# Kernel optimization log

Measured on AMD Instinct MI355X. Metric: run time of the kernel, lower is better.

## Reference

```python
import jax, jax.numpy as jnp
import numpy as np

MAX_ANTS = 16  # padded max draws per (batch, neuron); ragged draws masked with -1
BS, N_IN, N_OUT = 32, 4096, 4096


def setup_inputs() -> dict:
    key = jax.random.key(0)
    k1, k2 = jax.random.split(key)
    # integer ant counts per (batch, input neuron), in [0, MAX_ANTS)
    x = jax.random.randint(k1, (BS, N_IN), 0, MAX_ANTS, dtype=jnp.int32)
    # positive weights (original init is uniform 1/n_outputs; random positive is general)
    weights = jax.random.uniform(k2, (N_IN, N_OUT), dtype=jnp.float32, minval=0.01, maxval=1.0)
    return {"x": x, "weights": weights}


def reference(x, weights):
    """Vectorized equivalent of ACOLayer.forward.

    Original: for each batch b and input neuron i with count c = x[b, i] > 0,
    draw c iid categorical samples from row-normalized weights[i].
    Here: inverse-CDF sampling, padded to MAX_ANTS draws, invalid slots = -1.
    Returns int32 [bs, n_in, MAX_ANTS].
    """
    probs = weights / weights.sum(axis=1, keepdims=True)   # normalize()
    cdf = jnp.cumsum(probs, axis=1)                        # [n_in, n_out]
    bs, n_in = x.shape
    n_out = weights.shape[1]
    u = jax.random.uniform(jax.random.key(42), (bs, n_in, MAX_ANTS), dtype=weights.dtype)
    # group draws by input neuron so each row's CDF is searched once
    u_rows = u.transpose(1, 0, 2).reshape(n_in, bs * MAX_ANTS)  # [n_in, bs*MAX]
    idx = jax.vmap(jnp.searchsorted)(cdf, u_rows)               # inverse-CDF draw
    idx = jnp.minimum(idx, n_out - 1).astype(jnp.int32)
    idx = idx.reshape(n_in, bs, MAX_ANTS).transpose(1, 0, 2)    # [bs, n_in, MAX]
    valid = jnp.arange(MAX_ANTS, dtype=x.dtype)[None, None, :] < x[:, :, None]
    return jnp.where(valid, idx, -1)
```

## Files before the change

### kernel.cpp

```cpp
#include <hip/hip_runtime.h>
#include <stdint.h>


#define N_IN    4096
#define N_OUT   4096
#define BS      32
#define MAX_A   16
#define THREADS 256
#define HALF    1048576u

__device__ __forceinline__ int padi(int j) { return j + (j >> 5); }

__device__ __forceinline__ uint32_t rotl32(uint32_t x, uint32_t r) {
    return (x << r) | (x >> (32u - r));
}

__device__ __forceinline__ void threefry2x32_42(uint32_t x0, uint32_t x1,
                                                uint32_t& o0, uint32_t& o1) {
    const uint32_t k0 = 0u, k1 = 42u;
    const uint32_t k2 = k0 ^ k1 ^ 0x1BD11BDAu;
    x0 += k0; x1 += k1;
#define TF_R(r) { x0 += x1; x1 = rotl32(x1, (r)); x1 ^= x0; }
    TF_R(13) TF_R(15) TF_R(26) TF_R(6)
    x0 += k1; x1 += k2 + 1u;
    TF_R(17) TF_R(29) TF_R(16) TF_R(24)
    x0 += k2; x1 += k0 + 2u;
    TF_R(13) TF_R(15) TF_R(26) TF_R(6)
    x0 += k0; x1 += k1 + 3u;
    TF_R(17) TF_R(29) TF_R(16) TF_R(24)
    x0 += k1; x1 += k2 + 4u;
    TF_R(13) TF_R(15) TF_R(26) TF_R(6)
    x0 += k2; x1 += k0 + 5u;
#undef TF_R
    o0 = x0; o1 = x1;
}

__device__ __forceinline__ float bits_to_uniform(uint32_t b) {
    uint32_t f = (b >> 9) | 0x3f800000u;
    float r;
    __builtin_memcpy(&r, &f, 4);
    return r - 1.0f;
}

__device__ __forceinline__ int lower_bound_cdf(const float* cdf, float tval) {
    int lo = 0, hi = N_OUT;
    #pragma unroll
    for (int it = 0; it < 12; ++it) {
        int mid = (lo + hi) >> 1;
        if (cdf[padi(mid)] < tval) lo = mid + 1; else hi = mid;
    }
    return lo < N_OUT ? lo : N_OUT - 1;
}

__global__ __launch_bounds__(THREADS)
void aco_sample_kernel(const int* __restrict__ x,
                       const float* __restrict__ w,
                       int* __restrict__ out) {
    __shared__ float cdf[N_OUT + (N_OUT >> 5)];
    __shared__ float wsum[4];
    __shared__ int   xc[BS];

    const int row  = blockIdx.x;
    const int t    = threadIdx.x;
    const int lane = t & 63;
    const int wid  = t >> 6;

    const float4* wrow = (const float4*)(w + (size_t)row * N_OUT);
    float4 v0 = wrow[t * 4 + 0];
    float4 v1 = wrow[t * 4 + 1];
    float4 v2 = wrow[t * 4 + 2];
    float4 v3 = wrow[t * 4 + 3];

    if (t < BS) xc[t] = x[t * N_IN + row];

    float loc[16];
    {
        float s = 0.f;
        s += v0.x; loc[0]  = s;  s += v0.y; loc[1]  = s;
        s += v0.z; loc[2]  = s;  s += v0.w; loc[3]  = s;
        s += v1.x; loc[4]  = s;  s += v1.y; loc[5]  = s;
        s += v1.z; loc[6]  = s;  s += v1.w; loc[7]  = s;
        s += v2.x; loc[8]  = s;  s += v2.y; loc[9]  = s;
        s += v2.z; loc[10] = s;  s += v2.w; loc[11] = s;
        s += v3.x; loc[12] = s;  s += v3.y; loc[13] = s;
        s += v3.z; loc[14] = s;  s += v3.w; loc[15] = s;
    }
    const float my_total = loc[15];

    float incl = my_total;
    #pragma unroll
    for (int d = 1; d < 64; d <<= 1) {
        float n = __shfl_up(incl, d, 64);
        if (lane >= d) incl += n;
    }
    if (lane == 63) wsum[wid] = incl;
    __syncthreads();

    const float4 ws = *(const float4*)wsum;
    const float total = ws.x + ws.y + ws.z + ws.w;
    float wprefix = 0.f;
    if (wid > 0) wprefix += ws.x;
    if (wid > 1) wprefix += ws.y;
    if (wid > 2) wprefix += ws.z;
    const float chunk_prefix = wprefix + incl - my_total;

    {
        const int base = t * 16;
        #pragma unroll
        for (int m = 0; m < 16; ++m)
            cdf[padi(base + m)] = chunk_prefix + loc[m];
    }
    __syncthreads();

    const int b = t >> 4;
    const int a = t & 15;
    const uint32_t j0 = (uint32_t)(b * (N_IN * MAX_A) + row * MAX_A + a);
    const uint32_t j1 = j0 + HALF;

    uint32_t o0, o1, p0, p1;
    threefry2x32_42(0u, j0, o0, o1);
    threefry2x32_42(0u, j1, p0, p1);
    const float t0 = bits_to_uniform(o0 ^ o1) * total;
    const float t1 = bits_to_uniform(p0 ^ p1) * total;

    const int idx0 = lower_bound_cdf(cdf, t0);
    const int idx1 = lower_bound_cdf(cdf, t1);

    out[j0] = (a < xc[b])      ? idx0 : -1;
    out[j1] = (a < xc[b + 16]) ? idx1 : -1;
}

extern "C" void kernel_launch(void* const* d_in, const int* in_sizes, int n_in,
                              void* d_out, int out_size, void* d_ws, size_t ws_size,
                              hipStream_t stream) {
    const int*   x;
    const float* w;
    if (in_sizes[0] == BS * N_IN) { x = (const int*)d_in[0]; w = (const float*)d_in[1]; }
    else                          { x = (const int*)d_in[1]; w = (const float*)d_in[0]; }
    aco_sample_kernel<<<N_IN, THREADS, 0, stream>>>(x, w, (int*)d_out);
}
```

Before: 20.91 us.

## Hoist RNG before scan and guess-window binary search with fallback

Threefry random generation moves ahead of the weight prefix scan so its ALU work can overlap the global loads and block barriers. The CDF search now guesses an index from u*N_OUT, checks that the answer lies inside a ±64 window, and if so runs a 7-step search instead of 12. Otherwise it falls back to the full search, and the two draws' searches are interleaved. The window only holds when the CDF is close to uniform, which suits these near-uniform random weights. A failed check costs extra shared-memory reads and wave divergence.

```diff
diff --git a/kernel.cpp b/kernel.cpp
--- a/kernel.cpp
+++ b/kernel.cpp
@@ -8,6 +8,7 @@
 #define MAX_A   16
 #define THREADS 256
 #define HALF    1048576u
+#define WIN     64
 
 __device__ __forceinline__ int padi(int j) { return j + (j >> 5); }
 
@@ -42,16 +43,6 @@
     return r - 1.0f;
 }
 
-__device__ __forceinline__ int lower_bound_cdf(const float* cdf, float tval) {
-    int lo = 0, hi = N_OUT;
-    #pragma unroll
-    for (int it = 0; it < 12; ++it) {
-        int mid = (lo + hi) >> 1;
-        if (cdf[padi(mid)] < tval) lo = mid + 1; else hi = mid;
-    }
-    return lo < N_OUT ? lo : N_OUT - 1;
-}
-
 __global__ __launch_bounds__(THREADS)
 void aco_sample_kernel(const int* __restrict__ x,
                        const float* __restrict__ w,
@@ -72,6 +63,16 @@
     float4 v3 = wrow[t * 4 + 3];
 
     if (t < BS) xc[t] = x[t * N_IN + row];
+
+    const int bb = t >> 4;
+    const int aa = t & 15;
+    const uint32_t j0 = (uint32_t)(bb * (N_IN * MAX_A) + row * MAX_A + aa);
+    const uint32_t j1 = j0 + HALF;
+    uint32_t o0, o1, p0, p1;
+    threefry2x32_42(0u, j0, o0, o1);
+    threefry2x32_42(0u, j1, p0, p1);
+    const float u0 = bits_to_uniform(o0 ^ o1);
+    const float u1 = bits_to_uniform(p0 ^ p1);
 
     float loc[16];
     {
@@ -112,22 +113,48 @@
     }
     __syncthreads();
 
-    const int b = t >> 4;
-    const int a = t & 15;
-    const uint32_t j0 = (uint32_t)(b * (N_IN * MAX_A) + row * MAX_A + a);
-    const uint32_t j1 = j0 + HALF;
+    const float t0 = u0 * total;
+    const float t1 = u1 * total;
 
-    uint32_t o0, o1, p0, p1;
-    threefry2x32_42(0u, j0, o0, o1);
-    threefry2x32_42(0u, j1, p0, p1);
-    const float t0 = bits_to_uniform(o0 ^ o1) * total;
-    const float t1 = bits_to_uniform(p0 ^ p1) * total;
+    const int i0 = (int)(u0 * (float)N_OUT);
+    const int i1 = (int)(u1 * (float)N_OUT);
+    int lo0 = i0 - WIN; if (lo0 < 0) lo0 = 0;
+    int hi0 = i0 + WIN; if (hi0 > N_OUT) hi0 = N_OUT;
+    int lo1 = i1 - WIN; if (lo1 < 0) lo1 = 0;
+    int hi1 = i1 + WIN; if (hi1 > N_OUT) hi1 = N_OUT;
 
-    const int idx0 = lower_bound_cdf(cdf, t0);
-    const int idx1 = lower_bound_cdf(cdf, t1);
+    const bool ok0 = (lo0 == 0     || cdf[padi(lo0 - 1)] <  t0) &&
+                     (hi0 == N_OUT || cdf[padi(hi0 - 1)] >= t0);
+    const bool ok1 = (lo1 == 0     || cdf[padi(lo1 - 1)] <  t1) &&
+                     (hi1 == N_OUT || cdf[padi(hi1 - 1)] >= t1);
 
-    out[j0] = (a < xc[b])      ? idx0 : -1;
-    out[j1] = (a < xc[b + 16]) ? idx1 : -1;
+    if (ok0 && ok1) {
+        #pragma unroll
+        for (int it = 0; it < 7; ++it) {
+            const int m0 = (lo0 + hi0) >> 1;
+            const int m1 = (lo1 + hi1) >> 1;
+            const float f0 = cdf[padi(m0)];
+            const float f1 = cdf[padi(m1)];
+            if (f0 < t0) lo0 = m0 + 1; else hi0 = m0;
+            if (f1 < t1) lo1 = m1 + 1; else hi1 = m1;
+        }
+    } else {
+        lo0 = 0; hi0 = N_OUT; lo1 = 0; hi1 = N_OUT;
+        #pragma unroll
+        for (int it = 0; it < 12; ++it) {
+            const int m0 = (lo0 + hi0) >> 1;
+            const int m1 = (lo1 + hi1) >> 1;
+            const float f0 = cdf[padi(m0)];
+            const float f1 = cdf[padi(m1)];
+            if (f0 < t0) lo0 = m0 + 1; else hi0 = m0;
+            if (f1 < t1) lo1 = m1 + 1; else hi1 = m1;
+        }
+    }
+    const int idx0 = lo0 < N_OUT ? lo0 : N_OUT - 1;
+    const int idx1 = lo1 < N_OUT ? lo1 : N_OUT - 1;
+
+    out[j0] = (aa < xc[bb])      ? idx0 : -1;
+    out[j1] = (aa < xc[bb + 16]) ? idx1 : -1;
 }
 
 extern "C" void kernel_launch(void* const* d_in, const int* in_sizes, int n_in,
```

After: 19.96 us. 1.05x faster.

## Store CDF as packed fp16, halve threads, and use windowed binary search

Applied to the files above, without the earlier changes.

Halves block size to 128 threads, with each thread handling 32 weights and 4 draws. The per-row CDF is stored in shared memory as packed fp16 pairs rather than fp32. Draws are computed before the weight reduction, and the search first checks a ±64 window around the uniform-guess index, falling back to a full 12-step search. This cuts LDS footprint and search steps and raises occupancy, but fp16 CDF values (with round-toward-zero packing) lose precision, so sampled indices may differ from the fp32 reference near bucket boundaries. The window guess assumes roughly uniform weights, which holds only for the test distribution.

```diff
diff --git a/kernel.cpp b/kernel.cpp
--- a/kernel.cpp
+++ b/kernel.cpp
@@ -6,10 +6,13 @@
 #define N_OUT   4096
 #define BS      32
 #define MAX_A   16
-#define THREADS 256
+#define THREADS 128
 #define HALF    1048576u
+#define WIN     64
+#define NWORDS  (N_OUT / 2)
+#define PWORDS  (NWORDS + (NWORDS >> 5))
 
-__device__ __forceinline__ int padi(int j) { return j + (j >> 5); }
+__device__ __forceinline__ int padw(int wi) { return wi + (wi >> 5); }
 
 __device__ __forceinline__ uint32_t rotl32(uint32_t x, uint32_t r) {
     return (x << r) | (x >> (32u - r));
@@ -42,23 +45,29 @@
     return r - 1.0f;
 }
 
-__device__ __forceinline__ int lower_bound_cdf(const float* cdf, float tval) {
-    int lo = 0, hi = N_OUT;
-    #pragma unroll
-    for (int it = 0; it < 12; ++it) {
-        int mid = (lo + hi) >> 1;
-        if (cdf[padi(mid)] < tval) lo = mid + 1; else hi = mid;
-    }
-    return lo < N_OUT ? lo : N_OUT - 1;
+__device__ __forceinline__ uint32_t pack_h2(float a, float b) {
+    __fp16 v2[2];
+    *(decltype(__builtin_amdgcn_cvt_pkrtz(a, b))*)v2 = __builtin_amdgcn_cvt_pkrtz(a, b);
+    uint32_t u;
+    __builtin_memcpy(&u, v2, 4);
+    return u;
 }
 
-__global__ __launch_bounds__(THREADS)
+__device__ __forceinline__ float cdf_at(const uint32_t* cdfp, int e) {
+    const uint32_t wrd = cdfp[padw(e >> 1)];
+    const uint16_t h = (e & 1) ? (uint16_t)(wrd >> 16) : (uint16_t)(wrd & 0xffffu);
+    _Float16 v;
+    __builtin_memcpy(&v, &h, 2);
+    return (float)v;
+}
+
+__global__ __launch_bounds__(THREADS, 8)
 void aco_sample_kernel(const int* __restrict__ x,
                        const float* __restrict__ w,
                        int* __restrict__ out) {
-    __shared__ float cdf[N_OUT + (N_OUT >> 5)];
-    __shared__ float wsum[4];
-    __shared__ int   xc[BS];
+    __shared__ uint32_t cdfp[PWORDS];
+    __shared__ float    wsum[2];
+    __shared__ int      xc[BS];
 
     const int row  = blockIdx.x;
     const int t    = threadIdx.x;
@@ -66,26 +75,39 @@
     const int wid  = t >> 6;
 
     const float4* wrow = (const float4*)(w + (size_t)row * N_OUT);
-    float4 v0 = wrow[t * 4 + 0];
-    float4 v1 = wrow[t * 4 + 1];
-    float4 v2 = wrow[t * 4 + 2];
-    float4 v3 = wrow[t * 4 + 3];
+    float4 v0 = wrow[t * 8 + 0];
+    float4 v1 = wrow[t * 8 + 1];
+    float4 v2 = wrow[t * 8 + 2];
+    float4 v3 = wrow[t * 8 + 3];
+    float4 v4 = wrow[t * 8 + 4];
+    float4 v5 = wrow[t * 8 + 5];
+    float4 v6 = wrow[t * 8 + 6];
+    float4 v7 = wrow[t * 8 + 7];
 
     if (t < BS) xc[t] = x[t * N_IN + row];
 
-    float loc[16];
-    {
-        float s = 0.f;
-        s += v0.x; loc[0]  = s;  s += v0.y; loc[1]  = s;
-        s += v0.z; loc[2]  = s;  s += v0.w; loc[3]  = s;
-        s += v1.x; loc[4]  = s;  s += v1.y; loc[5]  = s;
-        s += v1.z; loc[6]  = s;  s += v1.w; loc[7]  = s;
-        s += v2.x; loc[8]  = s;  s += v2.y; loc[9]  = s;
-        s += v2.z; loc[10] = s;  s += v2.w; loc[11] = s;
-        s += v3.x; loc[12] = s;  s += v3.y; loc[13] = s;
-        s += v3.z; loc[14] = s;  s += v3.w; loc[15] = s;
+    const int bb = t >> 4;
+    const int aa = t & 15;
+    uint32_t jj[4];
+    float    uu[4];
+    #pragma unroll
+    for (int d = 0; d < 4; ++d) {
+        jj[d] = (uint32_t)((bb + 8 * d) * (N_IN * MAX_A) + row * MAX_A + aa);
+        uint32_t o0, o1;
+        threefry2x32_42(0u, jj[d], o0, o1);
+        uu[d] = bits_to_uniform(o0 ^ o1);
     }
-    const float my_total = loc[15];
+
+    float s = 0.f;
+    s += v0.x + v0.y + v0.z + v0.w;
+    s += v1.x + v1.y + v1.z + v1.w;
+    s += v2.x + v2.y + v2.z + v2.w;
+    s += v3.x + v3.y + v3.z + v3.w;
+    s += v4.x + v4.y + v4.z + v4.w;
+    s += v5.x + v5.y + v5.z + v5.w;
+    s += v6.x + v6.y + v6.z + v6.w;
+    s += v7.x + v7.y + v7.z + v7.w;
+    const float my_total = s;
 
     float incl = my_total;
     #pragma unroll
@@ -96,38 +118,68 @@
     if (lane == 63) wsum[wid] = incl;
     __syncthreads();
 
-    const float4 ws = *(const float4*)wsum;
-    const float total = ws.x + ws.y + ws.z + ws.w;
-    float wprefix = 0.f;
-    if (wid > 0) wprefix += ws.x;
-    if (wid > 1) wprefix += ws.y;
-    if (wid > 2) wprefix += ws.z;
-    const float chunk_prefix = wprefix + incl - my_total;
+    const float total = wsum[0] + wsum[1];
+    const float chunk_prefix = (wid ? wsum[0] : 0.f) + incl - my_total;
 
     {
-        const int base = t * 16;
-        #pragma unroll
-        for (int m = 0; m < 16; ++m)
-            cdf[padi(base + m)] = chunk_prefix + loc[m];
+        const int wbase = t * 16;
+        float r = chunk_prefix;
+        float f0, f1;
+#define EMIT(vv, wi_) \
+        f0 = r + vv.x; f1 = f0 + vv.y; \
+        cdfp[padw(wbase + (wi_))] = pack_h2(f0, f1); \
+        r = f1 + vv.z; f0 = r; r += vv.w; \
+        cdfp[padw(wbase + (wi_) + 1)] = pack_h2(f0, r);
+        EMIT(v0,  0) EMIT(v1,  2) EMIT(v2,  4) EMIT(v3,  6)
+        EMIT(v4,  8) EMIT(v5, 10) EMIT(v6, 12) EMIT(v7, 14)
+#undef EMIT
     }
     __syncthreads();
 
-    const int b = t >> 4;
-    const int a = t & 15;
-    const uint32_t j0 = (uint32_t)(b * (N_IN * MAX_A) + row * MAX_A + a);
-    const uint32_t j1 = j0 + HALF;
+    float tt[4];
+    int lo[4], hi[4];
+    bool allok = true;
+    #pragma unroll
+    for (int d = 0; d < 4; ++d) {
+        tt[d] = uu[d] * total;
+        const int i0 = (int)(uu[d] * (float)N_OUT);
+        int l = i0 - WIN; if (l < 0) l = 0;
+        int h = i0 + WIN; if (h > N_OUT) h = N_OUT;
+        const bool ok = (l == 0     || cdf_at(cdfp, l - 1) <  tt[d]) &&
+                        (h == N_OUT || cdf_at(cdfp, h - 1) >= tt[d]);
+        lo[d] = l; hi[d] = h;
+        allok = allok && ok;
+    }
 
-    uint32_t o0, o1, p0, p1;
-    threefry2x32_42(0u, j0, o0, o1);
-    threefry2x32_42(0u, j1, p0, p1);
-    const float t0 = bits_to_uniform(o0 ^ o1) * total;
-    const float t1 = bits_to_uniform(p0 ^ p1) * total;
+    if (allok) {
+        #pragma unroll
+        for (int it = 0; it < 7; ++it) {
+            #pragma unroll
+            for (int d = 0; d < 4; ++d) {
+                const int m = (lo[d] + hi[d]) >> 1;
+                const float f = cdf_at(cdfp, m);
+                if (f < tt[d]) lo[d] = m + 1; else hi[d] = m;
+            }
+        }
+    } else {
+        #pragma unroll
+        for (int d = 0; d < 4; ++d) { lo[d] = 0; hi[d] = N_OUT; }
+        #pragma unroll
+        for (int it = 0; it < 12; ++it) {
+            #pragma unroll
+            for (int d = 0; d < 4; ++d) {
+                const int m = (lo[d] + hi[d]) >> 1;
+                const float f = cdf_at(cdfp, m);
+                if (f < tt[d]) lo[d] = m + 1; else hi[d] = m;
+            }
+        }
+    }
 
-    const int idx0 = lower_bound_cdf(cdf, t0);
-    const int idx1 = lower_bound_cdf(cdf, t1);
-
-    out[j0] = (a < xc[b])      ? idx0 : -1;
-    out[j1] = (a < xc[b + 16]) ? idx1 : -1;
+    #pragma unroll
+    for (int d = 0; d < 4; ++d) {
+        const int idx = lo[d] < N_OUT ? lo[d] : N_OUT - 1;
+        out[jj[d]] = (aa < xc[bb + 8 * d]) ? idx : -1;
+    }
 }
 
 extern "C" void kernel_launch(void* const* d_in, const int* in_sizes, int n_in,
```

Measured after the change: 23.11 us. +10.5%, slower.
